# Kernel tuning notes

Measured on AMD Instinct MI355X. Metric: run time of the kernel, lower is better.

Reference implementation:

```python
import jax, jax.numpy as jnp
import numpy as np

H, D, L, G = 4, 32, 2, 512   # heads, head_dim, conv layers, num graphs
HC = H * D                    # hidden_channels = 128


def _mlp3(x, ws, bs):
    # PyG-style MLP, 3 layers, relu between (no act after last), dropout=0
    for i in range(3):
        x = x @ ws[i] + bs[i]
        if i < 2:
            x = jax.nn.relu(x)
    return x


def _attend(q_dst, k_src, v_src, edge, a_rel_et, m_rel_et, p_rel_et, n_dst):
    """One HGTConv edge-type: relation transform, per-dst segment softmax, scatter.
    q_dst: [Nd,H,D], k_src/v_src: [Ns,H,D], edge: [2,E] (src,dst)."""
    src, dst = edge[0], edge[1]
    k_t = jnp.einsum('nhd,hde->nhe', k_src, a_rel_et)   # relation-specific key
    v_t = jnp.einsum('nhd,hde->nhe', v_src, m_rel_et)   # relation-specific value
    alpha = (q_dst[dst] * k_t[src]).sum(-1) * p_rel_et / jnp.sqrt(jnp.float32(D))  # [E,H]
    amax = jax.ops.segment_max(alpha, dst, num_segments=n_dst)
    amax = jnp.where(jnp.isfinite(amax), amax, 0.0)      # nodes with no in-edges
    ex = jnp.exp(alpha - amax[dst])
    den = jax.ops.segment_sum(ex, dst, num_segments=n_dst)
    w = ex / den[dst]                                    # segment softmax weights
    out = jax.ops.segment_sum(v_t[src] * w[..., None], dst, num_segments=n_dst)
    return out.reshape(n_dst, HC)


def _forward(x_var, x_con, mlp_in_w, mlp_in_b,
             mlp_out_w0, mlp_out_b0, mlp_out_w1, mlp_out_b1, mlp_out_w2, mlp_out_b2,
             k_w, k_b, q_w, q_b, v_w, v_b, a_w, a_b, skip,
             a_rel, m_rel, p_rel, edge_vc, edge_cv, batch_var):
    Nv, Nc = x_var.shape[0], x_con.shape[0]
    # per-node-type input MLPs (nt 0 = variable, nt 1 = constraint)
    xs = [_mlp3(x_var, mlp_in_w[0], mlp_in_b[0]),
          _mlp3(x_con, mlp_in_w[1], mlp_in_b[1])]
    ns = [Nv, Nc]
    for l in range(L):  # HGTConv layers
        k = [(xs[t] @ k_w[l, t] + k_b[l, t]).reshape(ns[t], H, D) for t in (0, 1)]
        q = [(xs[t] @ q_w[l, t] + q_b[l, t]).reshape(ns[t], H, D) for t in (0, 1)]
        v = [(xs[t] @ v_w[l, t] + v_b[l, t]).reshape(ns[t], H, D) for t in (0, 1)]
        # edge type 0: variable -> constraint ; edge type 1: constraint -> variable
        agg_con = _attend(q[1], k[0], v[0], edge_vc, a_rel[l, 0], m_rel[l, 0], p_rel[l, 0], Nc)
        agg_var = _attend(q[0], k[1], v[1], edge_cv, a_rel[l, 1], m_rel[l, 1], p_rel[l, 1], Nv)
        # group='mean' over incoming edge types (one per dst type here), then a_lin + gated skip
        new_xs = []
        for t, agg in ((0, agg_var), (1, agg_con)):
            out = jax.nn.gelu(agg, approximate=False) @ a_w[l, t] + a_b[l, t]
            g = jax.nn.sigmoid(skip[l, t])
            new_xs.append(g * out + (1.0 - g) * xs[t])
        xs = new_xs
    # output head on 'variable' nodes: MLP -> softmax(dim=1) -> global mean pool
    logits = _mlp3(xs[0], [mlp_out_w0, mlp_out_w1, mlp_out_w2], [mlp_out_b0, mlp_out_b1, mlp_out_b2])
    probs = jax.nn.softmax(logits, axis=1)
    summ = jax.ops.segment_sum(probs, batch_var, num_segments=G)
    cnt = jax.ops.segment_sum(jnp.ones((xs[0].shape[0],), probs.dtype), batch_var, num_segments=G)
    return summ / jnp.maximum(cnt, 1.0)[:, None]


def setup_inputs() -> dict:
    key = jax.random.key(0)
    ks = jax.random.split(key, 24)
    Nv = Nc = 50000
    E = 400000
    s = 1.0 / np.sqrt(HC)  # fan-in scale for hidden-width linears
    sd = 1.0 / np.sqrt(D)
    inp = {
        'x_var': jax.random.normal(ks[0], (Nv, HC), jnp.float32),
        'x_con': jax.random.normal(ks[1], (Nc, HC), jnp.float32),
        'mlp_in_w': jax.random.normal(ks[2], (2, 3, HC, HC), jnp.float32) * s,
        'mlp_in_b': jnp.zeros((2, 3, HC), jnp.float32),
        'mlp_out_w0': jax.random.normal(ks[3], (HC, HC), jnp.float32) * s,
        'mlp_out_b0': jnp.zeros((HC,), jnp.float32),
        'mlp_out_w1': jax.random.normal(ks[4], (HC, HC), jnp.float32) * s,
        'mlp_out_b1': jnp.zeros((HC,), jnp.float32),
        'mlp_out_w2': jax.random.normal(ks[5], (HC, 2), jnp.float32) * s,
        'mlp_out_b2': jnp.zeros((2,), jnp.float32),
        'k_w': jax.random.normal(ks[6], (L, 2, HC, HC), jnp.float32) * s,
        'k_b': jnp.zeros((L, 2, HC), jnp.float32),
        'q_w': jax.random.normal(ks[7], (L, 2, HC, HC), jnp.float32) * s,
        'q_b': jnp.zeros((L, 2, HC), jnp.float32),
        'v_w': jax.random.normal(ks[8], (L, 2, HC, HC), jnp.float32) * s,
        'v_b': jnp.zeros((L, 2, HC), jnp.float32),
        'a_w': jax.random.normal(ks[9], (L, 2, HC, HC), jnp.float32) * s,
        'a_b': jnp.zeros((L, 2, HC), jnp.float32),
        'skip': jnp.ones((L, 2), jnp.float32),
        'a_rel': jax.random.normal(ks[10], (L, 2, H, D, D), jnp.float32) * sd,
        'm_rel': jax.random.normal(ks[11], (L, 2, H, D, D), jnp.float32) * sd,
        'p_rel': jnp.ones((L, 2, H), jnp.float32),
        'edge_vc': jnp.stack([jax.random.randint(ks[12], (E,), 0, Nv, jnp.int32),
                              jax.random.randint(ks[13], (E,), 0, Nc, jnp.int32)]),
        'edge_cv': jnp.stack([jax.random.randint(ks[14], (E,), 0, Nc, jnp.int32),
                              jax.random.randint(ks[15], (E,), 0, Nv, jnp.int32)]),
        'batch_var': jnp.sort(jax.random.randint(ks[16], (Nv,), 0, G, jnp.int32)),
    }
    return inp


def reference(x_var, x_con, mlp_in_w, mlp_in_b,
              mlp_out_w0, mlp_out_b0, mlp_out_w1, mlp_out_b1, mlp_out_w2, mlp_out_b2,
              k_w, k_b, q_w, q_b, v_w, v_b, a_w, a_b, skip,
              a_rel, m_rel, p_rel, edge_vc, edge_cv, batch_var):
    return _forward(x_var, x_con, mlp_in_w, mlp_in_b,
                    mlp_out_w0, mlp_out_b0, mlp_out_w1, mlp_out_b1, mlp_out_w2, mlp_out_b2,
                    k_w, k_b, q_w, q_b, v_w, v_b, a_w, a_b, skip,
                    a_rel, m_rel, p_rel, edge_vc, edge_cv, batch_var)
```

## Files before the change

kernel.cpp:

```cpp
#include <hip/hip_runtime.h>
#include <cstddef>
#include <cstdint>

typedef __attribute__((ext_vector_type(8))) short short8;
typedef __attribute__((ext_vector_type(4))) float float4v;
typedef __attribute__((ext_vector_type(2))) float float2v;
typedef __attribute__((ext_vector_type(2))) __bf16 bf162;

__device__ __forceinline__ float bf2f_lo(unsigned int u) {
    union { unsigned int i; float f; } v; v.i = u << 16; return v.f;
}
__device__ __forceinline__ float bf2f_hi(unsigned int u) {
    union { unsigned int i; float f; } v; v.i = u & 0xFFFF0000u; return v.f;
}
__device__ __forceinline__ unsigned short f2bf(float f) {
    union { float f; unsigned int i; } v; v.f = f;
    unsigned int x = v.i;
    unsigned int r = (x + 0x7FFFu + ((x >> 16) & 1u)) >> 16;
    return (unsigned short)r;
}
__device__ __forceinline__ float geluf(float x) {
    return 0.5f * x * (1.0f + erff(x * 0.70710678118654752f));
}
__device__ __forceinline__ float dot2bf(unsigned int a, unsigned int b, float c) {
#if defined(__has_builtin) && __has_builtin(__builtin_amdgcn_fdot2_f32_bf16)
    union U { unsigned int u; bf162 v; };
    U ua, ub; ua.u = a; ub.u = b;
    return __builtin_amdgcn_fdot2_f32_bf16(ua.v, ub.v, c, false);
#else
    return c + bf2f_lo(a) * bf2f_lo(b) + bf2f_hi(a) * bf2f_hi(b);
#endif
}
__device__ __forceinline__ unsigned int gate_pack(unsigned int nu, unsigned int ou,
                                                  float2v g2, float2v og2) {
    float2v n = {bf2f_lo(nu), bf2f_hi(nu)};
    float2v o = {bf2f_lo(ou), bf2f_hi(ou)};
    float2v r = n * g2 + o * og2;
    return (unsigned int)f2bf(r.x) | ((unsigned int)f2bf(r.y) << 16);
}

__global__ void k_zero(int* __restrict__ p, int n) {
    int i = blockIdx.x * 256 + threadIdx.x;
    if (i < n) p[i] = 0;
}

__global__ void k_swz(const float* __restrict__ mlp_in_w, const float* __restrict__ q_w,
                      const float* __restrict__ a_w, const float* __restrict__ mow0,
                      const float* __restrict__ mow1, const float* __restrict__ mow2,
                      const float* __restrict__ kw, const float* __restrict__ kb,
                      const float* __restrict__ vw, const float* __restrict__ vb,
                      const float* __restrict__ arel, const float* __restrict__ mrel,
                      const float* __restrict__ prel,
                      unsigned short* __restrict__ Wswz, float* __restrict__ Bkv) {
    int idx = blockIdx.y;
    int f = blockIdx.x * 256 + threadIdx.x;
    if (idx == 25) {
        if (f >= 1024) return;
        int lt = f >> 8, c = f & 255;
        int sec = c >> 7, cc = c & 127, h = cc >> 5, e = cc & 31;
        const float* B = sec ? vb : kb;
        const float* R = sec ? mrel : arel;
        float scale = sec ? 1.f : prel[lt * 4 + h] * 0.17677669529663687f;
        const float* rp = R + (size_t)(lt * 4 + h) * 1024 + e;
        const float* bp = B + lt * 128 + h * 32;
        float s = 0.f;
        #pragma unroll 8
        for (int d = 0; d < 32; ++d) s += bp[d] * rp[(size_t)d * 32];
        Bkv[lt * 256 + c] = s * scale;
        return;
    }
    if (f >= 16384) return;
    int j = f & 7, l = (f >> 3) & 63, t = (f >> 9) & 7, sb = f >> 12;
    int k = sb * 32 + (l >> 4) * 8 + j;
    int n = t * 16 + (l & 15);
    float val;
    if (idx < 6)        val = mlp_in_w[(size_t)idx * 16384 + (size_t)k * 128 + n];
    else if (idx < 10)  val = q_w[(size_t)(idx - 6) * 16384 + (size_t)k * 128 + n];
    else if (idx < 14)  val = a_w[(size_t)(idx - 10) * 16384 + (size_t)k * 128 + n];
    else if (idx == 14) val = mow0[(size_t)k * 128 + n];
    else if (idx == 15) val = mow1[(size_t)k * 128 + n];
    else if (idx < 24) {
        int u = idx - 16, lt = u >> 1, sec = u & 1;
        int h = n >> 5, e = n & 31;
        const float* W = sec ? vw : kw;
        const float* R = sec ? mrel : arel;
        float scale = sec ? 1.f : prel[lt * 4 + h] * 0.17677669529663687f;
        const float* rp = R + (size_t)(lt * 4 + h) * 1024 + e;
        const float* wp = W + (size_t)lt * 16384 + (size_t)k * 128 + h * 32;
        float s = 0.f;
        #pragma unroll 8
        for (int d = 0; d < 32; ++d) s += wp[d] * rp[(size_t)d * 32];
        val = s * scale;
    } else val = (n < 2) ? mow2[(size_t)k * 2 + n] : 0.f;
    Wswz[(size_t)idx * 16384 + f] = f2bf(val);
}

__device__ __forceinline__ void mfma32(const short8 av[4], const unsigned short* __restrict__ Bu,
                                       float4v acc[8]) {
    #pragma unroll
    for (int s = 0; s < 4; ++s)
        #pragma unroll
        for (int t = 0; t < 8; ++t) {
            short8 bv = *(const short8*)(Bu + (s * 8 + t) * 512);
            acc[t] = __builtin_amdgcn_mfma_f32_16x16x32_bf16(av[s], bv, acc[t], 0, 0, 0);
        }
}

__global__ __launch_bounds__(256) void k_mlp3qkv(
    const float* __restrict__ Xa, const float* __restrict__ Xb,
    const unsigned short* __restrict__ Wswz, const float* __restrict__ mlp_in_b,
    const float* __restrict__ q_b, const float* __restrict__ Bkv,
    unsigned short* __restrict__ curS, unsigned short* __restrict__ Qs,
    unsigned short* __restrict__ KVs, int NT, int Nv) {
    __shared__ unsigned short lds[4][16][136];
    const int lane = threadIdx.x & 63, wave = threadIdx.x >> 6;
    const int quad = lane >> 4, mrow = lane & 15;
    const int mbase = blockIdx.x * 64 + wave * 16;
    if (mbase >= NT) return;
    const bool first = mbase < Nv;
    const float* bs = mlp_in_b + (first ? 0 : 384);
    const int ub = first ? 0 : 3;
    const int lt = first ? 0 : 1;
    int r0 = mbase + mrow; if (r0 >= NT) r0 = NT - 1;
    const float* ap = ((r0 < Nv) ? (Xa + (size_t)r0 * 128)
                                 : (Xb + (size_t)(r0 - Nv) * 128)) + quad * 8;
    short8 av[4];
    #pragma unroll
    for (int s = 0; s < 4; ++s) {
        float4 f0 = *(const float4*)(ap + s * 32);
        float4 f1 = *(const float4*)(ap + s * 32 + 4);
        short8 a;
        a[0] = (short)f2bf(f0.x); a[1] = (short)f2bf(f0.y);
        a[2] = (short)f2bf(f0.z); a[3] = (short)f2bf(f0.w);
        a[4] = (short)f2bf(f1.x); a[5] = (short)f2bf(f1.y);
        a[6] = (short)f2bf(f1.z); a[7] = (short)f2bf(f1.w);
        av[s] = a;
    }
    #pragma unroll
    for (int layer = 0; layer < 3; ++layer) {
        const unsigned short* Bu = Wswz + (size_t)(ub + layer) * 16384 + lane * 8;
        float4v acc[8];
        #pragma unroll
        for (int t = 0; t < 8; ++t) acc[t] = (float4v){0.f, 0.f, 0.f, 0.f};
        mfma32(av, Bu, acc);
        const float* b = bs + layer * 128;
        bool relu = layer < 2;
        #pragma unroll
        for (int t = 0; t < 8; ++t) {
            int col = t * 16 + mrow;
            float bb = b[col];
            #pragma unroll
            for (int r = 0; r < 4; ++r) {
                float v = acc[t][r] + bb;
                if (relu) v = fmaxf(v, 0.f);
                lds[wave][quad * 4 + r][col] = f2bf(v);
            }
        }
        #pragma unroll
        for (int s = 0; s < 4; ++s)
            av[s] = *(const short8*)&lds[wave][mrow][s * 32 + quad * 8];
    }
    {
        int row = mbase + mrow;
        if (row < NT) {
            #pragma unroll
            for (int s = 0; s < 4; ++s)
                *(uint4*)(curS + (size_t)row * 128 + quad * 8 + s * 32) = *(uint4*)&av[s];
        }
    }
    #pragma unroll
    for (int u = 0; u < 3; ++u) {
        int unit = (u == 0) ? (6 + lt) : (16 + lt * 2 + (u - 1));
        const unsigned short* Bu = Wswz + (size_t)unit * 16384 + lane * 8;
        float4v acc[8];
        #pragma unroll
        for (int t = 0; t < 8; ++t) acc[t] = (float4v){0.f, 0.f, 0.f, 0.f};
        mfma32(av, Bu, acc);
        const float* bias = (u == 0) ? (q_b + lt * 128) : (Bkv + lt * 256 + (u - 1) * 128);
        unsigned short* C = (u == 0) ? Qs : KVs;
        const int ldC = (u == 0) ? 128 : 256;
        const int cb = (u == 0) ? 0 : (u - 1) * 128;
        #pragma unroll
        for (int t = 0; t < 8; ++t) {
            int col = t * 16 + mrow;
            float b = bias[col];
            #pragma unroll
            for (int r = 0; r < 4; ++r) {
                int row = mbase + quad * 4 + r;
                if (row < NT) C[(size_t)row * ldC + cb + col] = f2bf(acc[t][r] + b);
            }
        }
    }
}

__global__ __launch_bounds__(256) void k_alinqkv(
    const unsigned short* __restrict__ Aagg, const unsigned short* __restrict__ Wswz,
    const float* __restrict__ a_b, const float* __restrict__ skipP,
    const float* __restrict__ q_b, const float* __restrict__ Bkv,
    unsigned short* __restrict__ curS, unsigned short* __restrict__ Qs,
    unsigned short* __restrict__ KVs, int NT, int Nv, int l) {
    __shared__ unsigned short lds[4][16][136];
    const int lane = threadIdx.x & 63, wave = threadIdx.x >> 6;
    const int quad = lane >> 4, mrow = lane & 15;
    const int mbase = blockIdx.x * 64 + wave * 16;
    if (mbase >= NT) return;
    const int type = (mbase >= Nv) ? 1 : 0;
    const int ltA = l * 2 + type;
    const int ltQ = (l + 1) * 2 + type;
    int r0 = mbase + mrow; if (r0 >= NT) r0 = NT - 1;
    const unsigned short* ap = Aagg + (size_t)r0 * 128 + quad * 8;
    short8 av[4];
    #pragma unroll
    for (int s = 0; s < 4; ++s) av[s] = *(const short8*)(ap + s * 32);
    {
        const unsigned short* Bu = Wswz + (size_t)(10 + ltA) * 16384 + lane * 8;
        float4v acc[8];
        #pragma unroll
        for (int t = 0; t < 8; ++t) acc[t] = (float4v){0.f, 0.f, 0.f, 0.f};
        mfma32(av, Bu, acc);
        const float* b = a_b + ltA * 128;
        #pragma unroll
        for (int t = 0; t < 8; ++t) {
            int col = t * 16 + mrow;
            float bb = b[col];
            #pragma unroll
            for (int r = 0; r < 4; ++r)
                lds[wave][quad * 4 + r][col] = f2bf(acc[t][r] + bb);
        }
    }
    {
        float gg = 1.f / (1.f + __expf(-skipP[ltA]));
        float2v g2 = {gg, gg}, og2 = {1.f - gg, 1.f - gg};
        int row = mbase + mrow;
        bool ok = row < NT;
        size_t rbase = (size_t)(ok ? row : 0) * 128;
        #pragma unroll
        for (int s = 0; s < 4; ++s) {
            short8 nv = *(const short8*)&lds[wave][mrow][s * 32 + quad * 8];
            uint4 nu = *(uint4*)&nv;
            uint4 ou = *(const uint4*)(curS + rbase + quad * 8 + s * 32);
            uint4 res;
            res.x = gate_pack(nu.x, ou.x, g2, og2);
            res.y = gate_pack(nu.y, ou.y, g2, og2);
            res.z = gate_pack(nu.z, ou.z, g2, og2);
            res.w = gate_pack(nu.w, ou.w, g2, og2);
            if (ok) *(uint4*)(curS + (size_t)row * 128 + quad * 8 + s * 32) = res;
            av[s] = *(short8*)&res;
        }
    }
    #pragma unroll
    for (int u = 0; u < 3; ++u) {
        int unit = (u == 0) ? (6 + ltQ) : (16 + ltQ * 2 + (u - 1));
        const unsigned short* Bu = Wswz + (size_t)unit * 16384 + lane * 8;
        float4v acc[8];
        #pragma unroll
        for (int t = 0; t < 8; ++t) acc[t] = (float4v){0.f, 0.f, 0.f, 0.f};
        mfma32(av, Bu, acc);
        const float* bias = (u == 0) ? (q_b + ltQ * 128) : (Bkv + ltQ * 256 + (u - 1) * 128);
        unsigned short* C = (u == 0) ? Qs : KVs;
        const int ldC = (u == 0) ? 128 : 256;
        const int cb = (u == 0) ? 0 : (u - 1) * 128;
        #pragma unroll
        for (int t = 0; t < 8; ++t) {
            int col = t * 16 + mrow;
            float b = bias[col];
            #pragma unroll
            for (int r = 0; r < 4; ++r) {
                int row = mbase + quad * 4 + r;
                if (row < NT) C[(size_t)row * ldC + cb + col] = f2bf(acc[t][r] + b);
            }
        }
    }
}

__global__ __launch_bounds__(256) void k_alinhead(
    const unsigned short* __restrict__ Aagg, const unsigned short* __restrict__ Wswz,
    const float* __restrict__ a_b, const float* __restrict__ skipP,
    const unsigned short* __restrict__ curS,
    const float* __restrict__ mob0, const float* __restrict__ mob1,
    const float* __restrict__ mob2, const int* __restrict__ batch,
    int N, int G, float* __restrict__ gsum, float* __restrict__ gcnt) {
    __shared__ unsigned short lds[4][16][136];
    __shared__ float sb[64][3];
    const int lane = threadIdx.x & 63, wave = threadIdx.x >> 6;
    const int quad = lane >> 4, mrow = lane & 15;
    const int tix = threadIdx.x;
    for (int i = tix; i < 192; i += 256) ((float*)sb)[i] = 0.f;
    __syncthreads();
    const int mbase = blockIdx.x * 64 + wave * 16;
    int bbase = blockIdx.x * 64; if (bbase >= N) bbase = N - 1;
    const int bmin = batch[bbase];
    if (mbase < N) {
        int r0 = mbase + mrow; if (r0 >= N) r0 = N - 1;
        const unsigned short* ap = Aagg + (size_t)r0 * 128 + quad * 8;
        short8 av[4];
        #pragma unroll
        for (int s = 0; s < 4; ++s) av[s] = *(const short8*)(ap + s * 32);
        {
            const unsigned short* Bu = Wswz + (size_t)12 * 16384 + lane * 8;
            float4v acc[8];
            #pragma unroll
            for (int t = 0; t < 8; ++t) acc[t] = (float4v){0.f, 0.f, 0.f, 0.f};
            mfma32(av, Bu, acc);
            const float* b = a_b + 2 * 128;
            #pragma unroll
            for (int t = 0; t < 8; ++t) {
                int col = t * 16 + mrow;
                float bb = b[col];
                #pragma unroll
                for (int r = 0; r < 4; ++r)
                    lds[wave][quad * 4 + r][col] = f2bf(acc[t][r] + bb);
            }
        }
        {
            float gg = 1.f / (1.f + __expf(-skipP[2]));
            float2v g2 = {gg, gg}, og2 = {1.f - gg, 1.f - gg};
            size_t rbase = (size_t)r0 * 128;
            #pragma unroll
            for (int s = 0; s < 4; ++s) {
                short8 nv = *(const short8*)&lds[wave][mrow][s * 32 + quad * 8];
                uint4 nu = *(uint4*)&nv;
                uint4 ou = *(const uint4*)(curS + rbase + quad * 8 + s * 32);
                uint4 res;
                res.x = gate_pack(nu.x, ou.x, g2, og2);
                res.y = gate_pack(nu.y, ou.y, g2, og2);
                res.z = gate_pack(nu.z, ou.z, g2, og2);
                res.w = gate_pack(nu.w, ou.w, g2, og2);
                av[s] = *(short8*)&res;
            }
        }
        #pragma unroll
        for (int layer = 0; layer < 2; ++layer) {
            const unsigned short* Bu = Wswz + (size_t)(14 + layer) * 16384 + lane * 8;
            float4v acc[8];
            #pragma unroll
            for (int t = 0; t < 8; ++t) acc[t] = (float4v){0.f, 0.f, 0.f, 0.f};
            mfma32(av, Bu, acc);
            const float* b = layer ? mob1 : mob0;
            #pragma unroll
            for (int t = 0; t < 8; ++t) {
                int col = t * 16 + mrow;
                float bb = b[col];
                #pragma unroll
                for (int r = 0; r < 4; ++r)
                    lds[wave][quad * 4 + r][col] = f2bf(fmaxf(acc[t][r] + bb, 0.f));
            }
            #pragma unroll
            for (int s = 0; s < 4; ++s)
                av[s] = *(const short8*)&lds[wave][mrow][s * 32 + quad * 8];
        }
        float4v lg = (float4v){0.f, 0.f, 0.f, 0.f};
        #pragma unroll
        for (int s = 0; s < 4; ++s) {
            short8 bv = *(const short8*)(Wswz + (size_t)24 * 16384 + (size_t)(s * 8) * 512 + lane * 8);
            lg = __builtin_amdgcn_mfma_f32_16x16x32_bf16(av[s], bv, lg, 0, 0, 0);
        }
        float4v lgo;
        #pragma unroll
        for (int r = 0; r < 4; ++r) lgo[r] = __shfl_xor(lg[r], 1);
        if (mrow == 0) {
            #pragma unroll
            for (int r = 0; r < 4; ++r) {
                int row = mbase + quad * 4 + r;
                if (row < N) {
                    float l0 = lg[r] + mob2[0];
                    float l1 = lgo[r] + mob2[1];
                    float mm = fmaxf(l0, l1);
                    float e0 = __expf(l0 - mm), e1 = __expf(l1 - mm);
                    float inv = 1.f / (e0 + e1);
                    int b = batch[row];
                    int rel = b - bmin;
                    if (rel >= 0 && rel < 64) {
                        atomicAdd(&sb[rel][0], e0 * inv);
                        atomicAdd(&sb[rel][1], e1 * inv);
                        atomicAdd(&sb[rel][2], 1.f);
                    } else {
                        atomicAdd(&gsum[b * 2 + 0], e0 * inv);
                        atomicAdd(&gsum[b * 2 + 1], e1 * inv);
                        atomicAdd(&gcnt[b], 1.f);
                    }
                }
            }
        }
    }
    __syncthreads();
    for (int i = tix; i < 64; i += 256) {
        float c = sb[i][2];
        if (c != 0.f && bmin + i < G) {
            atomicAdd(&gsum[(bmin + i) * 2 + 0], sb[i][0]);
            atomicAdd(&gsum[(bmin + i) * 2 + 1], sb[i][1]);
            atomicAdd(&gcnt[bmin + i], c);
        }
    }
}

__global__ void k_hist2(const int* __restrict__ evc, const int* __restrict__ ecv, int E,
                        int* __restrict__ deg, int Nv) {
    int e = blockIdx.x * 256 + threadIdx.x;
    if (e >= E) return;
    if (blockIdx.y == 0) atomicAdd(&deg[Nv + evc[E + e]], 1);
    else                 atomicAdd(&deg[ecv[E + e]], 1);
}
__global__ void k_scan_block(const int* __restrict__ deg, int n, int* __restrict__ off,
                             int* __restrict__ partials) {
    __shared__ int s[256];
    int i = blockIdx.x * 256 + threadIdx.x;
    s[threadIdx.x] = (i < n) ? deg[i] : 0;
    __syncthreads();
    for (int d = 1; d < 256; d <<= 1) {
        int t = (threadIdx.x >= d) ? s[threadIdx.x - d] : 0;
        __syncthreads();
        s[threadIdx.x] += t;
        __syncthreads();
    }
    if (i < n) off[i + 1] = s[threadIdx.x];
    if (threadIdx.x == 255) partials[blockIdx.x] = s[255];
}
__global__ void k_scan_partials(int* __restrict__ partials, int nb) {
    __shared__ int s[512];
    s[threadIdx.x] = (threadIdx.x < nb) ? partials[threadIdx.x] : 0;
    __syncthreads();
    for (int d = 1; d < 512; d <<= 1) {
        int t = (threadIdx.x >= d) ? s[threadIdx.x - d] : 0;
        __syncthreads();
        s[threadIdx.x] += t;
        __syncthreads();
    }
    if (threadIdx.x < nb) partials[threadIdx.x] = s[threadIdx.x];
}
__global__ void k_scan_add(int* __restrict__ off, int* __restrict__ cur,
                           const int* __restrict__ partials, int n) {
    int i = blockIdx.x * 256 + threadIdx.x;
    if (i == 0) { off[0] = 0; cur[0] = 0; }
    if (i < n) {
        int b = i >> 8;
        int v = off[i + 1] + ((b > 0) ? partials[b - 1] : 0);
        off[i + 1] = v;
        cur[i + 1] = v;
    }
}
__global__ void k_scatter2(const int* __restrict__ evc, const int* __restrict__ ecv, int E,
                           int* __restrict__ cur, int Nv, int* __restrict__ srcAll) {
    int e = blockIdx.x * 256 + threadIdx.x;
    if (e >= E) return;
    if (blockIdx.y == 0) {
        int d = Nv + evc[E + e];
        int pos = atomicAdd(&cur[d], 1);
        srcAll[pos] = evc[e];
    } else {
        int d = ecv[E + e];
        int pos = atomicAdd(&cur[d], 1);
        srcAll[pos] = Nv + ecv[e];
    }
}

__global__ __launch_bounds__(256) void k_agg(
    const unsigned short* __restrict__ Q, const unsigned short* __restrict__ KV,
    const int* __restrict__ off, const int* __restrict__ csrc,
    unsigned short* __restrict__ out, int NT) {
    int dst = blockIdx.x * 4 + (threadIdx.x >> 6);
    int lane = threadIdx.x & 63;
    if (dst >= NT) return;
    const int g = lane >> 4, w = lane & 15;
    int2 se = *(const int2*)(off + dst);
    int s0 = se.x, s1 = se.y;
    uint4 qr = *(const uint4*)(Q + (size_t)dst * 128 + w * 8);
    float2v a0 = {0.f, 0.f}, a1 = {0.f, 0.f}, a2 = {0.f, 0.f}, a3 = {0.f, 0.f};
    float den = 0.f;
    int j = s0 + g;
    uint4 kr = {0, 0, 0, 0}, vr = {0, 0, 0, 0};
    bool have = j < s1;
    if (have) {
        const unsigned short* kv = KV + (size_t)csrc[j] * 256 + w * 8;
        kr = *(const uint4*)kv;
        vr = *(const uint4*)(kv + 128);
    }
    while (have) {
        int jn = j + 4;
        bool haveN = jn < s1;
        uint4 krn = kr, vrn = vr;
        if (haveN) {
            const unsigned short* kv = KV + (size_t)csrc[jn] * 256 + w * 8;
            krn = *(const uint4*)kv;
            vrn = *(const uint4*)(kv + 128);
        }
        float t = dot2bf(kr.x, qr.x, 0.f);
        t = dot2bf(kr.y, qr.y, t);
        t = dot2bf(kr.z, qr.z, t);
        t = dot2bf(kr.w, qr.w, t);
        t += __shfl_xor(t, 1);
        t += __shfl_xor(t, 2);
        t = fminf(fmaxf(t, -30.f), 30.f);
        float p = __expf(t);
        den += p;
        float2v pv = {p, p};
        a0 += pv * (float2v){bf2f_lo(vr.x), bf2f_hi(vr.x)};
        a1 += pv * (float2v){bf2f_lo(vr.y), bf2f_hi(vr.y)};
        a2 += pv * (float2v){bf2f_lo(vr.z), bf2f_hi(vr.z)};
        a3 += pv * (float2v){bf2f_lo(vr.w), bf2f_hi(vr.w)};
        kr = krn; vr = vrn; j = jn; have = haveN;
    }
    den += __shfl_xor(den, 16); den += __shfl_xor(den, 32);
    a0.x += __shfl_xor(a0.x, 16); a0.x += __shfl_xor(a0.x, 32);
    a0.y += __shfl_xor(a0.y, 16); a0.y += __shfl_xor(a0.y, 32);
    a1.x += __shfl_xor(a1.x, 16); a1.x += __shfl_xor(a1.x, 32);
    a1.y += __shfl_xor(a1.y, 16); a1.y += __shfl_xor(a1.y, 32);
    a2.x += __shfl_xor(a2.x, 16); a2.x += __shfl_xor(a2.x, 32);
    a2.y += __shfl_xor(a2.y, 16); a2.y += __shfl_xor(a2.y, 32);
    a3.x += __shfl_xor(a3.x, 16); a3.x += __shfl_xor(a3.x, 32);
    a3.y += __shfl_xor(a3.y, 16); a3.y += __shfl_xor(a3.y, 32);
    float inv = (s1 > s0) ? 1.f / den : 0.f;
    float2v r = a0;
    if (g == 1) r = a1;
    if (g == 2) r = a2;
    if (g == 3) r = a3;
    float r0 = geluf(r.x * inv), r1 = geluf(r.y * inv);
    unsigned int o = (unsigned int)f2bf(r0) | ((unsigned int)f2bf(r1) << 16);
    *(unsigned int*)(out + (size_t)dst * 128 + w * 8 + g * 2) = o;
}

__global__ void k_finalize(const float* __restrict__ gsum, const float* __restrict__ gcnt,
                           float* __restrict__ out, int n) {
    int i = blockIdx.x * 256 + threadIdx.x;
    if (i < n) out[i] = gsum[i] / fmaxf(gcnt[i >> 1], 1.f);
}

extern "C" void kernel_launch(void* const* d_in, const int* in_sizes, int n_in,
                              void* d_out, int out_size, void* d_ws, size_t ws_size,
                              hipStream_t stream) {
    const float* x_var    = (const float*)d_in[0];
    const float* x_con    = (const float*)d_in[1];
    const float* mlp_in_w = (const float*)d_in[2];
    const float* mlp_in_b = (const float*)d_in[3];
    const float* mow0 = (const float*)d_in[4];
    const float* mob0 = (const float*)d_in[5];
    const float* mow1 = (const float*)d_in[6];
    const float* mob1 = (const float*)d_in[7];
    const float* mow2 = (const float*)d_in[8];
    const float* mob2 = (const float*)d_in[9];
    const float* k_w  = (const float*)d_in[10];
    const float* k_b  = (const float*)d_in[11];
    const float* q_w  = (const float*)d_in[12];
    const float* q_b  = (const float*)d_in[13];
    const float* v_w  = (const float*)d_in[14];
    const float* v_b  = (const float*)d_in[15];
    const float* a_w  = (const float*)d_in[16];
    const float* a_b  = (const float*)d_in[17];
    const float* skipP = (const float*)d_in[18];
    const float* a_rel = (const float*)d_in[19];
    const float* m_rel = (const float*)d_in[20];
    const float* p_rel = (const float*)d_in[21];
    const int* edge_vc = (const int*)d_in[22];
    const int* edge_cv = (const int*)d_in[23];
    const int* batch   = (const int*)d_in[24];

    const int Nv = in_sizes[0] / 128;
    const int Nc = in_sizes[1] / 128;
    const int E  = in_sizes[22] / 2;
    const int G  = out_size / 2;
    const int NT = Nv + Nc;

    float* fbase = (float*)d_ws;
    size_t fo = 0;
    auto falloc = [&](size_t n) { float* p = fbase + fo; fo += n; return p; };
    float* Bkv  = falloc(4 * 256);
    float* gsum = falloc((size_t)G * 2);
    float* gcnt = falloc((size_t)G);

    unsigned short* bbase = (unsigned short*)(fbase + fo);
    size_t bo = 0;
    auto balloc = [&](size_t n) { unsigned short* p = bbase + bo; bo += n; return p; };
    unsigned short* Wswz = balloc((size_t)25 * 16384);
    unsigned short* curS = balloc((size_t)NT * 128);
    unsigned short* Qs   = balloc((size_t)NT * 128);
    unsigned short* KVs  = balloc((size_t)NT * 256);

    int* ibase = (int*)(bbase + bo);
    size_t io = 0;
    auto ialloc = [&](size_t n) { int* p = ibase + io; io += n; return p; };
    int* offAll = ialloc((size_t)NT + 1);
    int* curAll = ialloc((size_t)NT + 1);
    int* srcAll = ialloc((size_t)E * 2);
    int* deg    = ialloc((size_t)NT);
    int* partials = ialloc(512);

    size_t need = (char*)(ibase + io) - (char*)d_ws;
    if (need > ws_size) return;

    const int eb  = (E + 255) / 256;
    const int nzb = (NT + 255) / 256;
    const int gNT = (NT + 63) / 64;
    const int gNv = (Nv + 63) / 64;

    k_zero<<<nzb, 256, 0, stream>>>(deg, NT);
    k_hist2<<<dim3(eb, 2), 256, 0, stream>>>(edge_vc, edge_cv, E, deg, Nv);
    k_scan_block<<<nzb, 256, 0, stream>>>(deg, NT, offAll, partials);
    k_scan_partials<<<1, 512, 0, stream>>>(partials, nzb);
    k_scan_add<<<nzb, 256, 0, stream>>>(offAll, curAll, partials, NT);
    k_scatter2<<<dim3(eb, 2), 256, 0, stream>>>(edge_vc, edge_cv, E, curAll, Nv, srcAll);

    k_swz<<<dim3(64, 26), 256, 0, stream>>>(mlp_in_w, q_w, a_w, mow0, mow1, mow2,
                                            k_w, k_b, v_w, v_b, a_rel, m_rel, p_rel,
                                            Wswz, Bkv);
    k_zero<<<(G * 3 + 255) / 256, 256, 0, stream>>>((int*)gsum, G * 3);

    k_mlp3qkv<<<gNT, 256, 0, stream>>>(x_var, x_con, Wswz, mlp_in_b, q_b, Bkv,
                                       curS, Qs, KVs, NT, Nv);
    k_agg<<<(NT + 3) / 4, 256, 0, stream>>>(Qs, KVs, offAll, srcAll, Qs, NT);
    k_alinqkv<<<gNT, 256, 0, stream>>>(Qs, Wswz, a_b, skipP, q_b, Bkv,
                                       curS, Qs, KVs, NT, Nv, 0);
    k_agg<<<(NT + 3) / 4, 256, 0, stream>>>(Qs, KVs, offAll, srcAll, Qs, NT);
    k_alinhead<<<gNv, 256, 0, stream>>>(Qs, Wswz, a_b, skipP, curS,
                                        mob0, mob1, mob2, batch, Nv, G, gsum, gcnt);
    k_finalize<<<(G * 2 + 255) / 256, 256, 0, stream>>>(gsum, gcnt, (float*)d_out, G * 2);
}
```

Measured before the change: 525.4 us.

## Stage weight tiles in LDS per block and split blocks by node type

Each block now copies each 128x128 bf16 weight unit into shared memory cooperatively, and all four waves read MFMA B operands from LDS instead of each wave fetching them separately from global memory. Grid blocks are also partitioned by node type, so no block mixes variable and constraint rows, which keeps all waves in a block on the same weights. The cost is 32KB of extra LDS per block, which lowers occupancy, plus barriers around every weight stage that serialize the load and compute phases.

```diff
diff --git a/kernel.cpp b/kernel.cpp
--- a/kernel.cpp
+++ b/kernel.cpp
@@ -95,13 +95,22 @@
     Wswz[(size_t)idx * 16384 + f] = f2bf(val);
 }
 
-__device__ __forceinline__ void mfma32(const short8 av[4], const unsigned short* __restrict__ Bu,
-                                       float4v acc[8]) {
+__device__ __forceinline__ void stageB(const unsigned short* __restrict__ Wu,
+                                       unsigned short* __restrict__ Bst, int tid) {
+    #pragma unroll
+    for (int k = 0; k < 8; ++k)
+        ((uint4*)Bst)[tid + k * 256] = ((const uint4*)Wu)[tid + k * 256];
+}
+
+__device__ __forceinline__ void unit_ldst(const short8 av[4], const unsigned short* __restrict__ Bst,
+                                          int lane, float4v acc[8]) {
+    #pragma unroll
+    for (int t = 0; t < 8; ++t) acc[t] = (float4v){0.f, 0.f, 0.f, 0.f};
     #pragma unroll
     for (int s = 0; s < 4; ++s)
         #pragma unroll
         for (int t = 0; t < 8; ++t) {
-            short8 bv = *(const short8*)(Bu + (s * 8 + t) * 512);
+            short8 bv = *(const short8*)&Bst[(s * 8 + t) * 512 + lane * 8];
             acc[t] = __builtin_amdgcn_mfma_f32_16x16x32_bf16(av[s], bv, acc[t], 0, 0, 0);
         }
 }
@@ -111,19 +120,21 @@
     const unsigned short* __restrict__ Wswz, const float* __restrict__ mlp_in_b,
     const float* __restrict__ q_b, const float* __restrict__ Bkv,
     unsigned short* __restrict__ curS, unsigned short* __restrict__ Qs,
-    unsigned short* __restrict__ KVs, int NT, int Nv) {
-    __shared__ unsigned short lds[4][16][136];
-    const int lane = threadIdx.x & 63, wave = threadIdx.x >> 6;
+    unsigned short* __restrict__ KVs, int NT, int Nv, int Bv) {
+    __shared__ unsigned short Bst[16384];
+    __shared__ unsigned short tr[4][16][136];
+    const int tid = threadIdx.x;
+    const int lane = tid & 63, wave = tid >> 6;
     const int quad = lane >> 4, mrow = lane & 15;
-    const int mbase = blockIdx.x * 64 + wave * 16;
-    if (mbase >= NT) return;
-    const bool first = mbase < Nv;
-    const float* bs = mlp_in_b + (first ? 0 : 384);
-    const int ub = first ? 0 : 3;
-    const int lt = first ? 0 : 1;
-    int r0 = mbase + mrow; if (r0 >= NT) r0 = NT - 1;
-    const float* ap = ((r0 < Nv) ? (Xa + (size_t)r0 * 128)
-                                 : (Xb + (size_t)(r0 - Nv) * 128)) + quad * 8;
+    int bx = blockIdx.x;
+    int base, end, type;
+    if (bx < Bv) { base = bx * 64; end = Nv; type = 0; }
+    else         { base = Nv + (bx - Bv) * 64; end = NT; type = 1; }
+    const int mbase = base + wave * 16;
+    int r0 = mbase + mrow; if (r0 >= end) r0 = end - 1;
+    const bool rok = (mbase + mrow) < end;
+    const float* ap = (type == 0 ? Xa + (size_t)r0 * 128
+                                 : Xb + (size_t)(r0 - Nv) * 128) + quad * 8;
     short8 av[4];
     #pragma unroll
     for (int s = 0; s < 4; ++s) {
@@ -136,13 +147,14 @@
         a[6] = (short)f2bf(f1.z); a[7] = (short)f2bf(f1.w);
         av[s] = a;
     }
+    const float* bs = mlp_in_b + type * 384;
     #pragma unroll
     for (int layer = 0; layer < 3; ++layer) {
-        const unsigned short* Bu = Wswz + (size_t)(ub + layer) * 16384 + lane * 8;
+        __syncthreads();
+        stageB(Wswz + (size_t)(type * 3 + layer) * 16384, Bst, tid);
+        __syncthreads();
         float4v acc[8];
-        #pragma unroll
-        for (int t = 0; t < 8; ++t) acc[t] = (float4v){0.f, 0.f, 0.f, 0.f};
-        mfma32(av, Bu, acc);
+        unit_ldst(av, Bst, lane, acc);
         const float* b = bs + layer * 128;
         bool relu = layer < 2;
         #pragma unroll
@@ -153,30 +165,27 @@
             for (int r = 0; r < 4; ++r) {
                 float v = acc[t][r] + bb;
                 if (relu) v = fmaxf(v, 0.f);
-                lds[wave][quad * 4 + r][col] = f2bf(v);
+                tr[wave][quad * 4 + r][col] = f2bf(v);
             }
         }
         #pragma unroll
         for (int s = 0; s < 4; ++s)
-            av[s] = *(const short8*)&lds[wave][mrow][s * 32 + quad * 8];
-    }
-    {
-        int row = mbase + mrow;
-        if (row < NT) {
-            #pragma unroll
-            for (int s = 0; s < 4; ++s)
-                *(uint4*)(curS + (size_t)row * 128 + quad * 8 + s * 32) = *(uint4*)&av[s];
-        }
+            av[s] = *(const short8*)&tr[wave][mrow][s * 32 + quad * 8];
+    }
+    if (rok) {
+        #pragma unroll
+        for (int s = 0; s < 4; ++s)
+            *(uint4*)(curS + (size_t)r0 * 128 + quad * 8 + s * 32) = *(uint4*)&av[s];
     }
     #pragma unroll
     for (int u = 0; u < 3; ++u) {
-        int unit = (u == 0) ? (6 + lt) : (16 + lt * 2 + (u - 1));
-        const unsigned short* Bu = Wswz + (size_t)unit * 16384 + lane * 8;
+        int unit = (u == 0) ? (6 + type) : (16 + type * 2 + (u - 1));
+        __syncthreads();
+        stageB(Wswz + (size_t)unit * 16384, Bst, tid);
+        __syncthreads();
         float4v acc[8];
-        #pragma unroll
-        for (int t = 0; t < 8; ++t) acc[t] = (float4v){0.f, 0.f, 0.f, 0.f};
-        mfma32(av, Bu, acc);
-        const float* bias = (u == 0) ? (q_b + lt * 128) : (Bkv + lt * 256 + (u - 1) * 128);
+        unit_ldst(av, Bst, lane, acc);
+        const float* bias = (u == 0) ? (q_b + type * 128) : (Bkv + type * 256 + (u - 1) * 128);
         unsigned short* C = (u == 0) ? Qs : KVs;
         const int ldC = (u == 0) ? 128 : 256;
         const int cb = (u == 0) ? 0 : (u - 1) * 128;
@@ -187,7 +196,7 @@
             #pragma unroll
             for (int r = 0; r < 4; ++r) {
                 int row = mbase + quad * 4 + r;
-                if (row < NT) C[(size_t)row * ldC + cb + col] = f2bf(acc[t][r] + b);
+                if (row < end) C[(size_t)row * ldC + cb + col] = f2bf(acc[t][r] + b);
             }
         }
     }
@@ -198,26 +207,33 @@
     const float* __restrict__ a_b, const float* __restrict__ skipP,
     const float* __restrict__ q_b, const float* __restrict__ Bkv,
     unsigned short* __restrict__ curS, unsigned short* __restrict__ Qs,
-    unsigned short* __restrict__ KVs, int NT, int Nv, int l) {
-    __shared__ unsigned short lds[4][16][136];
-    const int lane = threadIdx.x & 63, wave = threadIdx.x >> 6;
+    unsigned short* __restrict__ KVs, int NT, int Nv, int Bv) {
+    __shared__ unsigned short Bst[16384];
+    __shared__ unsigned short tr[4][16][136];
+    const int tid = threadIdx.x;
+    const int lane = tid & 63, wave = tid >> 6;
     const int quad = lane >> 4, mrow = lane & 15;
-    const int mbase = blockIdx.x * 64 + wave * 16;
-    if (mbase >= NT) return;
-    const int type = (mbase >= Nv) ? 1 : 0;
-    const int ltA = l * 2 + type;
-    const int ltQ = (l + 1) * 2 + type;
-    int r0 = mbase + mrow; if (r0 >= NT) r0 = NT - 1;
-    const unsigned short* ap = Aagg + (size_t)r0 * 128 + quad * 8;
+    int bx = blockIdx.x;
+    int base, end, type;
+    if (bx < Bv) { base = bx * 64; end = Nv; type = 0; }
+    else         { base = Nv + (bx - Bv) * 64; end = NT; type = 1; }
+    const int mbase = base + wave * 16;
+    int r0 = mbase + mrow; if (r0 >= end) r0 = end - 1;
+    const bool rok = (mbase + mrow) < end;
+    const int ltA = type;
+    const int ltQ = 2 + type;
     short8 av[4];
-    #pragma unroll
-    for (int s = 0; s < 4; ++s) av[s] = *(const short8*)(ap + s * 32);
     {
-        const unsigned short* Bu = Wswz + (size_t)(10 + ltA) * 16384 + lane * 8;
+        const unsigned short* ap = Aagg + (size_t)r0 * 128 + quad * 8;
+        #pragma unroll
+        for (int s = 0; s < 4; ++s) av[s] = *(const short8*)(ap + s * 32);
+    }
+    {
+        __syncthreads();
+        stageB(Wswz + (size_t)(10 + ltA) * 16384, Bst, tid);
+        __syncthreads();
         float4v acc[8];
-        #pragma unroll
-        for (int t = 0; t < 8; ++t) acc[t] = (float4v){0.f, 0.f, 0.f, 0.f};
-        mfma32(av, Bu, acc);
+        unit_ldst(av, Bst, lane, acc);
         const float* b = a_b + ltA * 128;
         #pragma unroll
         for (int t = 0; t < 8; ++t) {
@@ -225,37 +241,34 @@
             float bb = b[col];
             #pragma unroll
             for (int r = 0; r < 4; ++r)
-                lds[wave][quad * 4 + r][col] = f2bf(acc[t][r] + bb);
+                tr[wave][quad * 4 + r][col] = f2bf(acc[t][r] + bb);
         }
     }
     {
         float gg = 1.f / (1.f + __expf(-skipP[ltA]));
         float2v g2 = {gg, gg}, og2 = {1.f - gg, 1.f - gg};
-        int row = mbase + mrow;
-        bool ok = row < NT;
-        size_t rbase = (size_t)(ok ? row : 0) * 128;
         #pragma unroll
         for (int s = 0; s < 4; ++s) {
-            short8 nv = *(const short8*)&lds[wave][mrow][s * 32 + quad * 8];
+            short8 nv = *(const short8*)&tr[wave][mrow][s * 32 + quad * 8];
             uint4 nu = *(uint4*)&nv;
-            uint4 ou = *(const uint4*)(curS + rbase + quad * 8 + s * 32);
+            uint4 ou = *(const uint4*)(curS + (size_t)r0 * 128 + quad * 8 + s * 32);
             uint4 res;
             res.x = gate_pack(nu.x, ou.x, g2, og2);
             res.y = gate_pack(nu.y, ou.y, g2, og2);
             res.z = gate_pack(nu.z, ou.z, g2, og2);
             res.w = gate_pack(nu.w, ou.w, g2, og2);
-            if (ok) *(uint4*)(curS + (size_t)row * 128 + quad * 8 + s * 32) = res;
+            if (rok) *(uint4*)(curS + (size_t)r0 * 128 + quad * 8 + s * 32) = res;
             av[s] = *(short8*)&res;
         }
     }
     #pragma unroll
     for (int u = 0; u < 3; ++u) {
         int unit = (u == 0) ? (6 + ltQ) : (16 + ltQ * 2 + (u - 1));
-        const unsigned short* Bu = Wswz + (size_t)unit * 16384 + lane * 8;
+        __syncthreads();
+        stageB(Wswz + (size_t)unit * 16384, Bst, tid);
+        __syncthreads();
         float4v acc[8];
-        #pragma unroll
-        for (int t = 0; t < 8; ++t) acc[t] = (float4v){0.f, 0.f, 0.f, 0.f};
-        mfma32(av, Bu, acc);
+        unit_ldst(av, Bst, lane, acc);
         const float* bias = (u == 0) ? (q_b + ltQ * 128) : (Bkv + ltQ * 256 + (u - 1) * 128);
         unsigned short* C = (u == 0) ? Qs : KVs;
         const int ldC = (u == 0) ? 128 : 256;
@@ -267,7 +280,7 @@
             #pragma unroll
             for (int r = 0; r < 4; ++r) {
                 int row = mbase + quad * 4 + r;
-                if (row < NT) C[(size_t)row * ldC + cb + col] = f2bf(acc[t][r] + b);
+                if (row < end) C[(size_t)row * ldC + cb + col] = f2bf(acc[t][r] + b);
             }
         }
     }
@@ -280,111 +293,113 @@
     const float* __restrict__ mob0, const float* __restrict__ mob1,
     const float* __restrict__ mob2, const int* __restrict__ batch,
     int N, int G, float* __restrict__ gsum, float* __restrict__ gcnt) {
-    __shared__ unsigned short lds[4][16][136];
+    __shared__ unsigned short Bst[16384];
+    __shared__ unsigned short tr[4][16][136];
     __shared__ float sb[64][3];
-    const int lane = threadIdx.x & 63, wave = threadIdx.x >> 6;
+    const int tid = threadIdx.x;
+    const int lane = tid & 63, wave = tid >> 6;
     const int quad = lane >> 4, mrow = lane & 15;
-    const int tix = threadIdx.x;
-    for (int i = tix; i < 192; i += 256) ((float*)sb)[i] = 0.f;
+    for (int i = tid; i < 192; i += 256) ((float*)sb)[i] = 0.f;
+    const int base = blockIdx.x * 64;
+    const int mbase = base + wave * 16;
+    int r0 = mbase + mrow; if (r0 >= N) r0 = N - 1;
+    const int bmin = batch[base < N ? base : N - 1];
+    short8 av[4];
+    {
+        const unsigned short* ap = Aagg + (size_t)r0 * 128 + quad * 8;
+        #pragma unroll
+        for (int s = 0; s < 4; ++s) av[s] = *(const short8*)(ap + s * 32);
+    }
+    {
+        __syncthreads();
+        stageB(Wswz + (size_t)12 * 16384, Bst, tid);
+        __syncthreads();
+        float4v acc[8];
+        unit_ldst(av, Bst, lane, acc);
+        const float* b = a_b + 2 * 128;
+        #pragma unroll
+        for (int t = 0; t < 8; ++t) {
+            int col = t * 16 + mrow;
+            float bb = b[col];
+            #pragma unroll
+            for (int r = 0; r < 4; ++r)
+                tr[wave][quad * 4 + r][col] = f2bf(acc[t][r] + bb);
+        }
+    }
+    {
+        float gg = 1.f / (1.f + __expf(-skipP[2]));
+        float2v g2 = {gg, gg}, og2 = {1.f - gg, 1.f - gg};
+        #pragma unroll
+        for (int s = 0; s < 4; ++s) {
+            short8 nv = *(const short8*)&tr[wave][mrow][s * 32 + quad * 8];
+            uint4 nu = *(uint4*)&nv;
+            uint4 ou = *(const uint4*)(curS + (size_t)r0 * 128 + quad * 8 + s * 32);
+            uint4 res;
+            res.x = gate_pack(nu.x, ou.x, g2, og2);
+            res.y = gate_pack(nu.y, ou.y, g2, og2);
+            res.z = gate_pack(nu.z, ou.z, g2, og2);
+            res.w = gate_pack(nu.w, ou.w, g2, og2);
+            av[s] = *(short8*)&res;
+        }
+    }
+    #pragma unroll
+    for (int layer = 0; layer < 2; ++layer) {
+        __syncthreads();
+        stageB(Wswz + (size_t)(14 + layer) * 16384, Bst, tid);
+        __syncthreads();
+        float4v acc[8];
+        unit_ldst(av, Bst, lane, acc);
+        const float* b = layer ? mob1 : mob0;
+        #pragma unroll
+        for (int t = 0; t < 8; ++t) {
+            int col = t * 16 + mrow;
+            float bb = b[col];
+            #pragma unroll
+            for (int r = 0; r < 4; ++r)
+                tr[wave][quad * 4 + r][col] = f2bf(fmaxf(acc[t][r] + bb, 0.f));
+        }
+        #pragma unroll
+        for (int s = 0; s < 4; ++s)
+            av[s] = *(const short8*)&tr[wave][mrow][s * 32 + quad * 8];
+    }
     __syncthreads();
-    const int mbase = blockIdx.x * 64 + wave * 16;
-    int bbase = blockIdx.x * 64; if (bbase >= N) bbase = N - 1;
-    const int bmin = batch[bbase];
-    if (mbase < N) {
-        int r0 = mbase + mrow; if (r0 >= N) r0 = N - 1;
-        const unsigned short* ap = Aagg + (size_t)r0 * 128 + quad * 8;
-        short8 av[4];
-        #pragma unroll
-        for (int s = 0; s < 4; ++s) av[s] = *(const short8*)(ap + s * 32);
-        {
-            const unsigned short* Bu = Wswz + (size_t)12 * 16384 + lane * 8;
-            float4v acc[8];
-            #pragma unroll
-            for (int t = 0; t < 8; ++t) acc[t] = (float4v){0.f, 0.f, 0.f, 0.f};
-            mfma32(av, Bu, acc);
-            const float* b = a_b + 2 * 128;
-            #pragma unroll
-            for (int t = 0; t < 8; ++t) {
-                int col = t * 16 + mrow;
-                float bb = b[col];
-                #pragma unroll
-                for (int r = 0; r < 4; ++r)
-                    lds[wave][quad * 4 + r][col] = f2bf(acc[t][r] + bb);
-            }
-        }
-        {
-            float gg = 1.f / (1.f + __expf(-skipP[2]));
-            float2v g2 = {gg, gg}, og2 = {1.f - gg, 1.f - gg};
-            size_t rbase = (size_t)r0 * 128;
-            #pragma unroll
-            for (int s = 0; s < 4; ++s) {
-                short8 nv = *(const short8*)&lds[wave][mrow][s * 32 + quad * 8];
-                uint4 nu = *(uint4*)&nv;
-                uint4 ou = *(const uint4*)(curS + rbase + quad * 8 + s * 32);
-                uint4 res;
-                res.x = gate_pack(nu.x, ou.x, g2, og2);
-                res.y = gate_pack(nu.y, ou.y, g2, og2);
-                res.z = gate_pack(nu.z, ou.z, g2, og2);
-                res.w = gate_pack(nu.w, ou.w, g2, og2);
-                av[s] = *(short8*)&res;
-            }
-        }
-        #pragma unroll
-        for (int layer = 0; layer < 2; ++layer) {
-            const unsigned short* Bu = Wswz + (size_t)(14 + layer) * 16384 + lane * 8;
-            float4v acc[8];
-            #pragma unroll
-            for (int t = 0; t < 8; ++t) acc[t] = (float4v){0.f, 0.f, 0.f, 0.f};
-            mfma32(av, Bu, acc);
-            const float* b = layer ? mob1 : mob0;
-            #pragma unroll
-            for (int t = 0; t < 8; ++t) {
-                int col = t * 16 + mrow;
-                float bb = b[col];
-                #pragma unroll
-                for (int r = 0; r < 4; ++r)
-                    lds[wave][quad * 4 + r][col] = f2bf(fmaxf(acc[t][r] + bb, 0.f));
-            }
-            #pragma unroll
-            for (int s = 0; s < 4; ++s)
-                av[s] = *(const short8*)&lds[wave][mrow][s * 32 + quad * 8];
-        }
-        float4v lg = (float4v){0.f, 0.f, 0.f, 0.f};
-        #pragma unroll
-        for (int s = 0; s < 4; ++s) {
-            short8 bv = *(const short8*)(Wswz + (size_t)24 * 16384 + (size_t)(s * 8) * 512 + lane * 8);
-            lg = __builtin_amdgcn_mfma_f32_16x16x32_bf16(av[s], bv, lg, 0, 0, 0);
-        }
-        float4v lgo;
-        #pragma unroll
-        for (int r = 0; r < 4; ++r) lgo[r] = __shfl_xor(lg[r], 1);
-        if (mrow == 0) {
-            #pragma unroll
-            for (int r = 0; r < 4; ++r) {
-                int row = mbase + quad * 4 + r;
-                if (row < N) {
-                    float l0 = lg[r] + mob2[0];
-                    float l1 = lgo[r] + mob2[1];
-                    float mm = fmaxf(l0, l1);
-                    float e0 = __expf(l0 - mm), e1 = __expf(l1 - mm);
-                    float inv = 1.f / (e0 + e1);
-                    int b = batch[row];
-                    int rel = b - bmin;
-                    if (rel >= 0 && rel < 64) {
-                        atomicAdd(&sb[rel][0], e0 * inv);
-                        atomicAdd(&sb[rel][1], e1 * inv);
-                        atomicAdd(&sb[rel][2], 1.f);
-                    } else {
-                        atomicAdd(&gsum[b * 2 + 0], e0 * inv);
-                        atomicAdd(&gsum[b * 2 + 1], e1 * inv);
-                        atomicAdd(&gcnt[b], 1.f);
-                    }
+    stageB(Wswz + (size_t)24 * 16384, Bst, tid);
+    __syncthreads();
+    float4v lg = (float4v){0.f, 0.f, 0.f, 0.f};
+    #pragma unroll
+    for (int s = 0; s < 4; ++s) {
+        short8 bv = *(const short8*)&Bst[(s * 8) * 512 + lane * 8];
+        lg = __builtin_amdgcn_mfma_f32_16x16x32_bf16(av[s], bv, lg, 0, 0, 0);
+    }
+    float4v lgo;
+    #pragma unroll
+    for (int r = 0; r < 4; ++r) lgo[r] = __shfl_xor(lg[r], 1);
+    if (mrow == 0) {
+        #pragma unroll
+        for (int r = 0; r < 4; ++r) {
+            int row = mbase + quad * 4 + r;
+            if (row < N) {
+                float l0 = lg[r] + mob2[0];
+                float l1 = lgo[r] + mob2[1];
+                float mm = fmaxf(l0, l1);
+                float e0 = __expf(l0 - mm), e1 = __expf(l1 - mm);
+                float inv = 1.f / (e0 + e1);
+                int b = batch[row];
+                int rel = b - bmin;
+                if (rel >= 0 && rel < 64) {
+                    atomicAdd(&sb[rel][0], e0 * inv);
+                    atomicAdd(&sb[rel][1], e1 * inv);
+                    atomicAdd(&sb[rel][2], 1.f);
+                } else {
+                    atomicAdd(&gsum[b * 2 + 0], e0 * inv);
+                    atomicAdd(&gsum[b * 2 + 1], e1 * inv);
+                    atomicAdd(&gcnt[b], 1.f);
                 }
             }
         }
     }
     __syncthreads();
-    for (int i = tix; i < 64; i += 256) {
+    for (int i = tid; i < 64; i += 256) {
         float c = sb[i][2];
         if (c != 0.f && bmin + i < G) {
             atomicAdd(&gsum[(bmin + i) * 2 + 0], sb[i][0]);
@@ -589,8 +604,8 @@
 
     const int eb  = (E + 255) / 256;
     const int nzb = (NT + 255) / 256;
-    const int gNT = (NT + 63) / 64;
-    const int gNv = (Nv + 63) / 64;
+    const int Bv  = (Nv + 63) / 64;
+    const int Bc  = (Nc + 63) / 64;
 
     k_zero<<<nzb, 256, 0, stream>>>(deg, NT);
     k_hist2<<<dim3(eb, 2), 256, 0, stream>>>(edge_vc, edge_cv, E, deg, Nv);
@@ -604,13 +619,13 @@
                                             Wswz, Bkv);
     k_zero<<<(G * 3 + 255) / 256, 256, 0, stream>>>((int*)gsum, G * 3);
 
-    k_mlp3qkv<<<gNT, 256, 0, stream>>>(x_var, x_con, Wswz, mlp_in_b, q_b, Bkv,
-                                       curS, Qs, KVs, NT, Nv);
+    k_mlp3qkv<<<Bv + Bc, 256, 0, stream>>>(x_var, x_con, Wswz, mlp_in_b, q_b, Bkv,
+                                           curS, Qs, KVs, NT, Nv, Bv);
     k_agg<<<(NT + 3) / 4, 256, 0, stream>>>(Qs, KVs, offAll, srcAll, Qs, NT);
-    k_alinqkv<<<gNT, 256, 0, stream>>>(Qs, Wswz, a_b, skipP, q_b, Bkv,
-                                       curS, Qs, KVs, NT, Nv, 0);
+    k_alinqkv<<<Bv + Bc, 256, 0, stream>>>(Qs, Wswz, a_b, skipP, q_b, Bkv,
+                                           curS, Qs, KVs, NT, Nv, Bv);
     k_agg<<<(NT + 3) / 4, 256, 0, stream>>>(Qs, KVs, offAll, srcAll, Qs, NT);
-    k_alinhead<<<gNv, 256, 0, stream>>>(Qs, Wswz, a_b, skipP, curS,
-                                        mob0, mob1, mob2, batch, Nv, G, gsum, gcnt);
+    k_alinhead<<<Bv, 256, 0, stream>>>(Qs, Wswz, a_b, skipP, curS,
+                                       mob0, mob1, mob2, batch, Nv, G, gsum, gcnt);
     k_finalize<<<(G * 2 + 255) / 256, 256, 0, stream>>>(gsum, gcnt, (float*)d_out, G * 2);
 }
```

Result: faster. 508.5 us (-3.2%).
